# Optimization experiments

Measured on AMD Instinct MI355X. Metric: run time of the kernel, lower is better.

## Reference

```python
import jax, jax.numpy as jnp
import numpy as np

ROW_OFF, COL_OFF = 85, 80  # paste offsets from Model.pad

def setup_inputs() -> dict:
    key = jax.random.key(0)
    k1, k2 = jax.random.split(key)
    img = jax.random.normal(k1, (64, 3, 416, 416), dtype=jnp.float32)
    # zero out a chunk so the !=0 mask is non-trivial
    img = img.at[:, :, :100, :100].set(0.0)
    image_ref = jax.random.uniform(k2, (1, 3, 608, 608), dtype=jnp.float32)
    return {"img": img, "image_ref": image_ref}

def reference(img, image_ref):
    # img: [B,3,h,w] rendered frames; image_ref: [1,3,H,W] padded/resized reference
    B, C, h, w = img.shape
    H, W = image_ref.shape[2:]
    out = jnp.broadcast_to(image_ref, (B, C, H, W))
    region = jax.lax.dynamic_slice(out, (0, 0, ROW_OFF, COL_OFF), (B, C, h, w))
    mask = (img[:, 2:3, :, :] != 0.0)  # [B,1,h,w], broadcast over channels
    composited = jnp.where(mask, img, region)
    out = jax.lax.dynamic_update_slice(out, composited, (0, 0, ROW_OFF, COL_OFF))
    return out
```

## Files before the change

### kernel.cpp

```cpp
#include <hip/hip_runtime.h>

#define BATCH   64
#define CH      3
#define H_OUT   608
#define W_OUT   608
#define H_IN    416
#define W_IN    416
#define ROW_OFF 85
#define COL_OFF 80

#define W4_OUT  (W_OUT / 4)
#define W4_IN   (W_IN / 4)
#define PLANE4  (H_OUT * W4_OUT)
#define IPLANE4 (H_IN * W4_IN)

__global__ __launch_bounds__(256)
void composite_kernel(const float4* __restrict__ img,
                      const float4* __restrict__ ref,
                      float4* __restrict__ out)
{
    const int i = blockIdx.x * 256 + threadIdx.x;
    const int c = blockIdx.y;
    const int b = blockIdx.z;

    const int y  = i / W4_OUT;
    const int x4 = i - y * W4_OUT;

    const float4 r = ref[c * PLANE4 + i];
    float4 o = r;

    const int yy = y - ROW_OFF;
    const int xx = x4 * 4 - COL_OFF;
    if (yy >= 0 && yy < H_IN && xx >= 0 && xx < W_IN) {
        const int base = yy * W4_IN + (xx >> 2);
        const float4 v = img[(b * CH + c) * IPLANE4 + base];
        const float4 m = img[(b * CH + 2) * IPLANE4 + base];
        o.x = (m.x != 0.0f) ? v.x : r.x;
        o.y = (m.y != 0.0f) ? v.y : r.y;
        o.z = (m.z != 0.0f) ? v.z : r.z;
        o.w = (m.w != 0.0f) ? v.w : r.w;
    }

    out[(b * CH + c) * PLANE4 + i] = o;
}

extern "C" void kernel_launch(void* const* d_in, const int* in_sizes, int n_in,
                              void* d_out, int out_size, void* d_ws, size_t ws_size,
                              hipStream_t stream) {
    const float4* img = (const float4*)d_in[0];
    const float4* ref = (const float4*)d_in[1];
    float4* out = (float4*)d_out;

    dim3 grid(PLANE4 / 256, CH, BATCH);
    composite_kernel<<<grid, 256, 0, stream>>>(img, ref, out);
}
```

Measured before the change: 386.9 us.

## Process all channels and a chunk of batches per thread to reuse mask and ref

Each thread now handles all three channels for four consecutive batch items. The reference pixels are loaded once and the mask channel is read once per batch rather than once per channel. This removes redundant mask and reference loads and gives each thread more independent memory operations. The cost is a smaller grid and more registers per thread.

New measurement: 384.4 us. About the same (-0.7%).

```diff
diff --git a/kernel.cpp b/kernel.cpp
--- a/kernel.cpp
+++ b/kernel.cpp
@@ -14,34 +14,58 @@
 #define PLANE4  (H_OUT * W4_OUT)
 #define IPLANE4 (H_IN * W4_IN)
 
+#define BCHUNK  4
+
+#define SEL(o, m, v, r) \
+    o.x = (m.x != 0.0f) ? v.x : r.x; \
+    o.y = (m.y != 0.0f) ? v.y : r.y; \
+    o.z = (m.z != 0.0f) ? v.z : r.z; \
+    o.w = (m.w != 0.0f) ? v.w : r.w;
+
 __global__ __launch_bounds__(256)
 void composite_kernel(const float4* __restrict__ img,
                       const float4* __restrict__ ref,
                       float4* __restrict__ out)
 {
-    const int i = blockIdx.x * 256 + threadIdx.x;
-    const int c = blockIdx.y;
-    const int b = blockIdx.z;
+    const int i  = blockIdx.x * 256 + threadIdx.x;
+    const int b0 = blockIdx.y * BCHUNK;
 
     const int y  = i / W4_OUT;
     const int x4 = i - y * W4_OUT;
 
-    const float4 r = ref[c * PLANE4 + i];
-    float4 o = r;
+    const float4 r0 = ref[0 * PLANE4 + i];
+    const float4 r1 = ref[1 * PLANE4 + i];
+    const float4 r2 = ref[2 * PLANE4 + i];
 
     const int yy = y - ROW_OFF;
     const int xx = x4 * 4 - COL_OFF;
-    if (yy >= 0 && yy < H_IN && xx >= 0 && xx < W_IN) {
+    const bool inw = (yy >= 0 && yy < H_IN && xx >= 0 && xx < W_IN);
+
+    if (inw) {
         const int base = yy * W4_IN + (xx >> 2);
-        const float4 v = img[(b * CH + c) * IPLANE4 + base];
-        const float4 m = img[(b * CH + 2) * IPLANE4 + base];
-        o.x = (m.x != 0.0f) ? v.x : r.x;
-        o.y = (m.y != 0.0f) ? v.y : r.y;
-        o.z = (m.z != 0.0f) ? v.z : r.z;
-        o.w = (m.w != 0.0f) ? v.w : r.w;
+        #pragma unroll
+        for (int j = 0; j < BCHUNK; ++j) {
+            const int b = b0 + j;
+            const float4 v0 = img[(b * CH + 0) * IPLANE4 + base];
+            const float4 v1 = img[(b * CH + 1) * IPLANE4 + base];
+            const float4 m  = img[(b * CH + 2) * IPLANE4 + base];
+            float4 o0, o1, o2;
+            SEL(o0, m, v0, r0)
+            SEL(o1, m, v1, r1)
+            SEL(o2, m, m,  r2)
+            out[(b * CH + 0) * PLANE4 + i] = o0;
+            out[(b * CH + 1) * PLANE4 + i] = o1;
+            out[(b * CH + 2) * PLANE4 + i] = o2;
+        }
+    } else {
+        #pragma unroll
+        for (int j = 0; j < BCHUNK; ++j) {
+            const int b = b0 + j;
+            out[(b * CH + 0) * PLANE4 + i] = r0;
+            out[(b * CH + 1) * PLANE4 + i] = r1;
+            out[(b * CH + 2) * PLANE4 + i] = r2;
+        }
     }
-
-    out[(b * CH + c) * PLANE4 + i] = o;
 }
 
 extern "C" void kernel_launch(void* const* d_in, const int* in_sizes, int n_in,
@@ -51,6 +75,6 @@
     const float4* ref = (const float4*)d_in[1];
     float4* out = (float4*)d_out;
 
-    dim3 grid(PLANE4 / 256, CH, BATCH);
+    dim3 grid(PLANE4 / 256, BATCH / BCHUNK);
     composite_kernel<<<grid, 256, 0, stream>>>(img, ref, out);
 }
```
